# Optimization experiments

Measured on AMD Instinct MI355X. Metric: run time of the kernel, lower is better.

## Reference

```python
import jax, jax.numpy as jnp
import numpy as np

N_NODES = 50000
N_FEAT = 128
N_HIDDEN = 256
N_CLASSES = 1
N_EDGES = 800000


def gcn_layer(x, src, dst, W, b, n_nodes):
    """GCNConv: D^-1/2 (A + I) D^-1/2 X W + b, via gather-scatter over edges."""
    h = x @ W  # [N, out]
    # add self loops
    loop = jnp.arange(n_nodes, dtype=src.dtype)
    s = jnp.concatenate([src, loop])
    d = jnp.concatenate([dst, loop])
    deg = jax.ops.segment_sum(jnp.ones_like(d, dtype=h.dtype), d, num_segments=n_nodes)
    inv_sqrt = jax.lax.rsqrt(jnp.maximum(deg, 1.0))
    norm = inv_sqrt[s] * inv_sqrt[d]  # [E+N]
    msgs = h[s] * norm[:, None]       # gather: [E+N, out]
    out = jax.ops.segment_sum(msgs, d, num_segments=n_nodes)  # scatter-add
    return out + b


def setup_inputs() -> dict:
    key = jax.random.key(0)
    k1, k2, k3, k4 = jax.random.split(key, 4)
    x = jax.random.normal(k1, (N_NODES, N_FEAT), dtype=jnp.float32)
    edge_index = jax.random.randint(k2, (2, N_EDGES), 0, N_NODES, dtype=jnp.int32)
    s1 = 1.0 / np.sqrt(N_FEAT)
    s2 = 1.0 / np.sqrt(N_HIDDEN)
    W1 = jax.random.uniform(k3, (N_FEAT, N_HIDDEN), jnp.float32, -s1, s1)
    b1 = jnp.zeros((N_HIDDEN,), jnp.float32)
    W2 = jax.random.uniform(k4, (N_HIDDEN, N_CLASSES), jnp.float32, -s2, s2)
    b2 = jnp.zeros((N_CLASSES,), jnp.float32)
    return {"x": x, "edge_index": edge_index, "W1": W1, "b1": b1, "W2": W2, "b2": b2}


def reference(x, edge_index, W1, b1, W2, b2):
    src, dst = edge_index[0], edge_index[1]
    n = x.shape[0]
    h = gcn_layer(x, src, dst, W1, b1, n)
    h = jax.nn.relu(h)  # dropout=0.0 -> identity
    out = gcn_layer(h, src, dst, W2, b2, n)
    return out  # [N, n_classes]
```

## Files before the change

kernel.cpp:

```cpp
#include <hip/hip_runtime.h>

typedef unsigned int uint;
typedef unsigned short ushort;
typedef __attribute__((ext_vector_type(8))) short short8;
typedef __attribute__((ext_vector_type(4))) float f32x4;

#define CAP   64
#define BM16  16
#define STR   68
#define NPB   192
#define NBIN  261
#define CAPB  4096
#define EPB   4096

__device__ __forceinline__ float bf_lo(uint p) { return __uint_as_float(p << 16); }
__device__ __forceinline__ float bf_hi(uint p) { return __uint_as_float(p & 0xffff0000u); }
__device__ __forceinline__ uint rne_lo(uint u) { return (u + 0x7fffu + ((u >> 16) & 1u)) >> 16; }
__device__ __forceinline__ uint rne_hi(uint u) { return (u + 0x7fffu + ((u >> 16) & 1u)) & 0xffff0000u; }

__global__ __launch_bounds__(1024) void k_part(
    const int* __restrict__ src, const int* __restrict__ dst,
    int* __restrict__ binCnt, uint* __restrict__ binData, int E) {
  __shared__ int hist[NBIN];
  __shared__ int base[NBIN];
  int t = threadIdx.x;
  for (int i = t; i < NBIN; i += 1024) hist[i] = 0;
  __syncthreads();
  int s[4], d[4], b[4];
  bool v[4];
#pragma unroll
  for (int j = 0; j < 4; ++j) {
    int e = blockIdx.x * EPB + j * 1024 + t;
    v[j] = e < E;
    if (v[j]) {
      s[j] = src[e];
      d[j] = dst[e];
      b[j] = d[j] / NPB;
      atomicAdd(&hist[b[j]], 1);
    }
  }
  __syncthreads();
  for (int i = t; i < NBIN; i += 1024) {
    int h = hist[i];
    base[i] = h ? atomicAdd(&binCnt[i], h) : 0;
    hist[i] = 0;
  }
  __syncthreads();
#pragma unroll
  for (int j = 0; j < 4; ++j) {
    if (v[j]) {
      int r = atomicAdd(&hist[b[j]], 1);
      int idx = base[b[j]] + r;
      if (idx < CAPB)
        binData[b[j] * CAPB + idx] = (uint)s[j] | ((uint)d[j] << 16);
    }
  }
}

__global__ __launch_bounds__(1024) void k_bucketize(
    const uint* __restrict__ binData, const int* __restrict__ binCnt,
    ushort* __restrict__ col, int* __restrict__ cnt, int N) {
  __shared__ ushort col_l[NPB * CAP];
  __shared__ int cnt_l[NPB];
  int b = blockIdx.x, t = threadIdx.x;
  int lo = b * NPB;
  for (int i = t; i < NPB; i += 1024) cnt_l[i] = 0;
  __syncthreads();
  int m = min(binCnt[b], CAPB);
  const uint* bd = &binData[b * CAPB];
  for (int e = t; e < m; e += 1024) {
    uint pr = bd[e];
    int sv = pr & 0xffffu;
    int dl = (int)(pr >> 16) - lo;
    int p = atomicAdd(&cnt_l[dl], 1);
    if (p < CAP) col_l[dl * CAP + p] = (ushort)sv;
  }
  __syncthreads();
  int nh = min(NPB, N - lo);
  if (nh <= 0) return;
  for (int i = t; i < nh; i += 1024) cnt[lo + i] = cnt_l[i];
  uint* cg = (uint*)(col + (size_t)lo * CAP);
  const uint* cl = (const uint*)col_l;
  int nu = nh * (CAP / 2);
  for (int i = t; i < nu; i += 1024) cg[i] = cl[i];
}

__global__ void k_prep2(const float2* __restrict__ x2, const int* __restrict__ cnt,
                        uint* __restrict__ xs, float* __restrict__ inv,
                        const float* __restrict__ W1, uint* __restrict__ wpack,
                        int N, int nconv) {
  int gid = blockIdx.x * blockDim.x + threadIdx.x;
  if (gid < 4096) {
    int kk = gid >> 10, rem = gid & 1023, ntile = rem >> 6, ln = rem & 63;
    int quad = ln >> 4, nn = ntile * 16 + (ln & 15);
    uint d[4];
#pragma unroll
    for (int jp = 0; jp < 4; ++jp) {
      int k = kk * 32 + quad * 8 + 2 * jp;
      uint lov = rne_lo(__float_as_uint(W1[k * 256 + nn]));
      uint hiv = rne_hi(__float_as_uint(W1[(k + 1) * 256 + nn]));
      d[jp] = lov | hiv;
    }
    *(uint4*)&wpack[gid * 4] = make_uint4(d[0], d[1], d[2], d[3]);
  } else if (gid < 4096 + N) {
    int i = gid - 4096;
    inv[i] = rsqrtf((float)(cnt[i] + 1));
  } else if (gid < 4096 + N + nconv) {
    int cid = gid - 4096 - N;
    int node = cid >> 6;
    float invd = rsqrtf((float)(cnt[node] + 1));
    float2 f = x2[cid];
    xs[cid] = rne_lo(__float_as_uint(invd * f.x)) | rne_hi(__float_as_uint(invd * f.y));
  }
}

__global__ __launch_bounds__(256, 2) void k_agg_gemm(
    const uint* __restrict__ xs, const ushort* __restrict__ col,
    const int* __restrict__ cnt, const float* __restrict__ inv,
    const uint* __restrict__ wpack, const float* __restrict__ b1,
    const float* __restrict__ W2, float* __restrict__ cz, int N) {
  __shared__ uint As[BM16 * STR];
  __shared__ float red[64];
  int t = threadIdx.x, wave = t >> 6, lane = t & 63;
  int m0 = blockIdx.x * BM16;

  for (int rr = 0; rr < 4; ++rr) {
    int m = wave * 4 + rr;
    int node = m0 + m;
    float2 acc = make_float2(0.f, 0.f);
    if (node < N) {
      uint pd = xs[(size_t)node * 64 + lane];
      acc.x = bf_lo(pd);
      acc.y = bf_hi(pd);
      int e = min(cnt[node], CAP);
      int ce = (int)col[node * CAP + lane];
      int p = 0;
      for (; p + 15 < e; p += 16) {
        uint pv[16];
#pragma unroll
        for (int j = 0; j < 16; ++j) {
          int s = __shfl(ce, p + j);
          pv[j] = xs[(size_t)s * 64 + lane];
        }
#pragma unroll
        for (int j = 0; j < 16; ++j) { acc.x += bf_lo(pv[j]); acc.y += bf_hi(pv[j]); }
      }
      for (; p + 3 < e; p += 4) {
        uint pv[4];
#pragma unroll
        for (int j = 0; j < 4; ++j) {
          int s = __shfl(ce, p + j);
          pv[j] = xs[(size_t)s * 64 + lane];
        }
#pragma unroll
        for (int j = 0; j < 4; ++j) { acc.x += bf_lo(pv[j]); acc.y += bf_hi(pv[j]); }
      }
      for (; p < e; ++p) {
        int s = __shfl(ce, p);
        uint p0 = xs[(size_t)s * 64 + lane];
        acc.x += bf_lo(p0); acc.y += bf_hi(p0);
      }
      float invd = inv[node];
      acc.x *= invd;
      acc.y *= invd;
    }
    As[m * STR + lane] = rne_lo(__float_as_uint(acc.x)) | rne_hi(__float_as_uint(acc.y));
  }
  __syncthreads();

  int quad = lane >> 4, mrow = lane & 15;
  f32x4 acc[4];
#pragma unroll
  for (int nt = 0; nt < 4; ++nt) acc[nt] = (f32x4){0.f, 0.f, 0.f, 0.f};
#pragma unroll
  for (int kk = 0; kk < 4; ++kk) {
    short8 af = *(const short8*)&As[mrow * STR + kk * 16 + quad * 4];
#pragma unroll
    for (int nt = 0; nt < 4; ++nt) {
      int ntile = wave * 4 + nt;
      short8 bf = *(const short8*)&wpack[((kk * 16 + ntile) * 64 + lane) * 4];
      acc[nt] = __builtin_amdgcn_mfma_f32_16x16x32_bf16(af, bf, acc[nt], 0, 0, 0);
    }
  }

  float partial[4] = {0.f, 0.f, 0.f, 0.f};
#pragma unroll
  for (int nt = 0; nt < 4; ++nt) {
    int c = (wave * 4 + nt) * 16 + mrow;
    float b1c = b1[c], w2c = W2[c];
#pragma unroll
    for (int r = 0; r < 4; ++r) {
      float h = fmaxf(acc[nt][r] + b1c, 0.f);
      partial[r] = fmaf(h, w2c, partial[r]);
    }
  }
#pragma unroll
  for (int r = 0; r < 4; ++r) {
    float p = partial[r];
    p += __shfl_xor(p, 1); p += __shfl_xor(p, 2);
    p += __shfl_xor(p, 4); p += __shfl_xor(p, 8);
    if (mrow == 0) red[wave * 16 + quad * 4 + r] = p;
  }
  __syncthreads();
  if (t < 16) {
    int node = m0 + t;
    if (node < N) {
      float s = red[t] + red[16 + t] + red[32 + t] + red[48 + t];
      cz[node] = inv[node] * s;
    }
  }
}

__global__ void k_agg2(const ushort* __restrict__ col, const int* __restrict__ cnt,
                       const float* __restrict__ cz, const float* __restrict__ b2,
                       float* __restrict__ out, int N) {
  int g = blockIdx.x * blockDim.x + threadIdx.x;
  int node = g >> 2, q = g & 3;
  if (node >= N) return;
  int e = min(cnt[node], CAP);
  float acc = (q == 0) ? cz[node] : 0.f;
  const ushort* cp = &col[node * CAP];
  for (int p = q; p < e; p += 4) acc += cz[cp[p]];
  acc += __shfl_xor(acc, 1);
  acc += __shfl_xor(acc, 2);
  if (q == 0) out[node] = rsqrtf((float)(cnt[node] + 1)) * acc + b2[0];
}

extern "C" void kernel_launch(void* const* d_in, const int* in_sizes, int n_in,
                              void* d_out, int out_size, void* d_ws, size_t ws_size,
                              hipStream_t stream) {
  const float2* x2 = (const float2*)d_in[0];
  const int*    ei = (const int*)d_in[1];
  const float*  W1 = (const float*)d_in[2];
  const float*  b1 = (const float*)d_in[3];
  const float*  W2 = (const float*)d_in[4];
  const float*  b2 = (const float*)d_in[5];
  int N = in_sizes[0] / 128;
  int E = in_sizes[1] / 2;
  const int* src = ei;
  const int* dst = ei + E;
  float* out = (float*)d_out;

  char* w = (char*)d_ws;
  size_t o = 0;
  auto carve = [&](size_t bytes) { char* p = w + o; o += (bytes + 255) & ~(size_t)255; return p; };
  int*    binCnt  = (int*)   carve((size_t)NBIN * 4);
  int*    cnt     = (int*)   carve((size_t)N * 4);
  uint*   binData = (uint*)  carve((size_t)NBIN * CAPB * 4);
  ushort* col     = (ushort*)carve((size_t)N * CAP * 2);
  uint*   xs      = (uint*)  carve((size_t)N * 64 * 4);
  float*  inv     = (float*) carve((size_t)N * 4);
  uint*   wpack   = (uint*)  carve(16384 * 4);
  float*  cz      = (float*) carve((size_t)N * 4);

  hipMemsetAsync(binCnt, 0, (size_t)NBIN * sizeof(int), stream);

  int nblk_p = (E + EPB - 1) / EPB;
  k_part<<<nblk_p, 1024, 0, stream>>>(src, dst, binCnt, binData, E);

  k_bucketize<<<NBIN, 1024, 0, stream>>>(binData, binCnt, col, cnt, N);

  int nconv = N * 64;
  int tprep = 4096 + N + nconv;
  k_prep2<<<(tprep + 255) / 256, 256, 0, stream>>>(x2, cnt, xs, inv, W1, wpack, N, nconv);

  k_agg_gemm<<<(N + BM16 - 1) / BM16, 256, 0, stream>>>(
      xs, col, cnt, inv, wpack, b1, W2, cz, N);

  long long tot2 = (long long)N * 4;
  k_agg2<<<(int)((tot2 + 255) / 256), 256, 0, stream>>>(col, cnt, cz, b2, out, N);
}
```

Measured before the change: 144.3 us.

## Fold prep kernel into partition/bucketize and interleave gathers across four nodes

Removes the separate prep kernel. W1 packing moves into the edge-partition kernel, while the degree inverse and the scaled bf16 conversion of x move into the bucketize kernel, which already holds per-node counts in shared memory. The aggregation loop now gathers neighbours for all four of a wave's nodes together in chunks of eight, which keeps more loads in flight, and occupancy is raised to 3 blocks per CU. The cost is extra padded loads for nodes with uneven degree, more register pressure from the interleaving, and zeroing of the shared column buffer.

```diff
diff --git a/kernel.cpp b/kernel.cpp
--- a/kernel.cpp
+++ b/kernel.cpp
@@ -20,10 +20,27 @@
 
 __global__ __launch_bounds__(1024) void k_part(
     const int* __restrict__ src, const int* __restrict__ dst,
-    int* __restrict__ binCnt, uint* __restrict__ binData, int E) {
+    int* __restrict__ binCnt, uint* __restrict__ binData, int E,
+    const float* __restrict__ W1, uint* __restrict__ wpack) {
   __shared__ int hist[NBIN];
   __shared__ int base[NBIN];
   int t = threadIdx.x;
+
+  int gid = blockIdx.x * 1024 + t;
+  if (gid < 4096) {
+    int kk = gid >> 10, rem = gid & 1023, ntile = rem >> 6, ln = rem & 63;
+    int quad = ln >> 4, nn = ntile * 16 + (ln & 15);
+    uint d[4];
+#pragma unroll
+    for (int jp = 0; jp < 4; ++jp) {
+      int k = kk * 32 + quad * 8 + 2 * jp;
+      uint lov = rne_lo(__float_as_uint(W1[k * 256 + nn]));
+      uint hiv = rne_hi(__float_as_uint(W1[(k + 1) * 256 + nn]));
+      d[jp] = lov | hiv;
+    }
+    *(uint4*)&wpack[gid * 4] = make_uint4(d[0], d[1], d[2], d[3]);
+  }
+
   for (int i = t; i < NBIN; i += 1024) hist[i] = 0;
   __syncthreads();
   int s[4], d[4], b[4];
@@ -59,12 +76,15 @@
 
 __global__ __launch_bounds__(1024) void k_bucketize(
     const uint* __restrict__ binData, const int* __restrict__ binCnt,
-    ushort* __restrict__ col, int* __restrict__ cnt, int N) {
+    ushort* __restrict__ col, int* __restrict__ cnt, int N,
+    const float2* __restrict__ x2, uint* __restrict__ xs, float* __restrict__ inv) {
   __shared__ ushort col_l[NPB * CAP];
   __shared__ int cnt_l[NPB];
   int b = blockIdx.x, t = threadIdx.x;
   int lo = b * NPB;
   for (int i = t; i < NPB; i += 1024) cnt_l[i] = 0;
+  uint* clz = (uint*)col_l;
+  for (int i = t; i < NPB * (CAP / 2); i += 1024) clz[i] = 0;
   __syncthreads();
   int m = min(binCnt[b], CAPB);
   const uint* bd = &binData[b * CAPB];
@@ -78,43 +98,26 @@
   __syncthreads();
   int nh = min(NPB, N - lo);
   if (nh <= 0) return;
-  for (int i = t; i < nh; i += 1024) cnt[lo + i] = cnt_l[i];
+  for (int i = t; i < nh; i += 1024) {
+    int c = cnt_l[i];
+    cnt[lo + i] = c;
+    inv[lo + i] = rsqrtf((float)(c + 1));
+  }
   uint* cg = (uint*)(col + (size_t)lo * CAP);
   const uint* cl = (const uint*)col_l;
   int nu = nh * (CAP / 2);
   for (int i = t; i < nu; i += 1024) cg[i] = cl[i];
-}
-
-__global__ void k_prep2(const float2* __restrict__ x2, const int* __restrict__ cnt,
-                        uint* __restrict__ xs, float* __restrict__ inv,
-                        const float* __restrict__ W1, uint* __restrict__ wpack,
-                        int N, int nconv) {
-  int gid = blockIdx.x * blockDim.x + threadIdx.x;
-  if (gid < 4096) {
-    int kk = gid >> 10, rem = gid & 1023, ntile = rem >> 6, ln = rem & 63;
-    int quad = ln >> 4, nn = ntile * 16 + (ln & 15);
-    uint d[4];
-#pragma unroll
-    for (int jp = 0; jp < 4; ++jp) {
-      int k = kk * 32 + quad * 8 + 2 * jp;
-      uint lov = rne_lo(__float_as_uint(W1[k * 256 + nn]));
-      uint hiv = rne_hi(__float_as_uint(W1[(k + 1) * 256 + nn]));
-      d[jp] = lov | hiv;
-    }
-    *(uint4*)&wpack[gid * 4] = make_uint4(d[0], d[1], d[2], d[3]);
-  } else if (gid < 4096 + N) {
-    int i = gid - 4096;
-    inv[i] = rsqrtf((float)(cnt[i] + 1));
-  } else if (gid < 4096 + N + nconv) {
-    int cid = gid - 4096 - N;
-    int node = cid >> 6;
-    float invd = rsqrtf((float)(cnt[node] + 1));
-    float2 f = x2[cid];
-    xs[cid] = rne_lo(__float_as_uint(invd * f.x)) | rne_hi(__float_as_uint(invd * f.y));
-  }
-}
-
-__global__ __launch_bounds__(256, 2) void k_agg_gemm(
+  int nc = nh << 6;
+  const float2* xb = x2 + ((size_t)lo << 6);
+  uint* xo = xs + ((size_t)lo << 6);
+  for (int i = t; i < nc; i += 1024) {
+    float iv = rsqrtf((float)(cnt_l[i >> 6] + 1));
+    float2 f = xb[i];
+    xo[i] = rne_lo(__float_as_uint(iv * f.x)) | rne_hi(__float_as_uint(iv * f.y));
+  }
+}
+
+__global__ __launch_bounds__(256, 3) void k_agg_gemm(
     const uint* __restrict__ xs, const ushort* __restrict__ col,
     const int* __restrict__ cnt, const float* __restrict__ inv,
     const uint* __restrict__ wpack, const float* __restrict__ b1,
@@ -124,47 +127,56 @@
   int t = threadIdx.x, wave = t >> 6, lane = t & 63;
   int m0 = blockIdx.x * BM16;
 
-  for (int rr = 0; rr < 4; ++rr) {
-    int m = wave * 4 + rr;
-    int node = m0 + m;
-    float2 acc = make_float2(0.f, 0.f);
+  int e4[4], ce4[4];
+  float2 ac[4];
+  float invd[4];
+#pragma unroll
+  for (int r = 0; r < 4; ++r) {
+    int node = m0 + wave * 4 + r;
     if (node < N) {
       uint pd = xs[(size_t)node * 64 + lane];
-      acc.x = bf_lo(pd);
-      acc.y = bf_hi(pd);
-      int e = min(cnt[node], CAP);
-      int ce = (int)col[node * CAP + lane];
-      int p = 0;
-      for (; p + 15 < e; p += 16) {
-        uint pv[16];
-#pragma unroll
-        for (int j = 0; j < 16; ++j) {
-          int s = __shfl(ce, p + j);
-          pv[j] = xs[(size_t)s * 64 + lane];
+      ac[r].x = bf_lo(pd);
+      ac[r].y = bf_hi(pd);
+      e4[r] = min(cnt[node], CAP);
+      ce4[r] = (int)col[(size_t)node * CAP + lane];
+      invd[r] = inv[node];
+    } else {
+      e4[r] = 0; ce4[r] = 0; invd[r] = 0.f;
+      ac[r] = make_float2(0.f, 0.f);
+    }
+  }
+  int emax = max(max(e4[0], e4[1]), max(e4[2], e4[3]));
+  for (int p = 0; p < emax; p += 8) {
+    uint pv[4][8];
+#pragma unroll
+    for (int r = 0; r < 4; ++r) {
+      if (p < e4[r]) {
+#pragma unroll
+        for (int j = 0; j < 8; ++j) {
+          int s = __shfl(ce4[r], p + j);
+          pv[r][j] = xs[(size_t)s * 64 + lane];
         }
-#pragma unroll
-        for (int j = 0; j < 16; ++j) { acc.x += bf_lo(pv[j]); acc.y += bf_hi(pv[j]); }
       }
-      for (; p + 3 < e; p += 4) {
-        uint pv[4];
-#pragma unroll
-        for (int j = 0; j < 4; ++j) {
-          int s = __shfl(ce, p + j);
-          pv[j] = xs[(size_t)s * 64 + lane];
+    }
+#pragma unroll
+    for (int r = 0; r < 4; ++r) {
+      if (p < e4[r]) {
+        int lim = e4[r] - p;
+#pragma unroll
+        for (int j = 0; j < 8; ++j) {
+          uint v = (j < lim) ? pv[r][j] : 0u;
+          ac[r].x += bf_lo(v);
+          ac[r].y += bf_hi(v);
         }
-#pragma unroll
-        for (int j = 0; j < 4; ++j) { acc.x += bf_lo(pv[j]); acc.y += bf_hi(pv[j]); }
       }
-      for (; p < e; ++p) {
-        int s = __shfl(ce, p);
-        uint p0 = xs[(size_t)s * 64 + lane];
-        acc.x += bf_lo(p0); acc.y += bf_hi(p0);
-      }
-      float invd = inv[node];
-      acc.x *= invd;
-      acc.y *= invd;
-    }
-    As[m * STR + lane] = rne_lo(__float_as_uint(acc.x)) | rne_hi(__float_as_uint(acc.y));
+    }
+  }
+#pragma unroll
+  for (int r = 0; r < 4; ++r) {
+    float axx = ac[r].x * invd[r];
+    float ayy = ac[r].y * invd[r];
+    As[(wave * 4 + r) * STR + lane] =
+        rne_lo(__float_as_uint(axx)) | rne_hi(__float_as_uint(ayy));
   }
   __syncthreads();
 
@@ -256,13 +268,9 @@
   hipMemsetAsync(binCnt, 0, (size_t)NBIN * sizeof(int), stream);
 
   int nblk_p = (E + EPB - 1) / EPB;
-  k_part<<<nblk_p, 1024, 0, stream>>>(src, dst, binCnt, binData, E);
-
-  k_bucketize<<<NBIN, 1024, 0, stream>>>(binData, binCnt, col, cnt, N);
-
-  int nconv = N * 64;
-  int tprep = 4096 + N + nconv;
-  k_prep2<<<(tprep + 255) / 256, 256, 0, stream>>>(x2, cnt, xs, inv, W1, wpack, N, nconv);
+  k_part<<<nblk_p, 1024, 0, stream>>>(src, dst, binCnt, binData, E, W1, wpack);
+
+  k_bucketize<<<NBIN, 1024, 0, stream>>>(binData, binCnt, col, cnt, N, x2, xs, inv);
 
   k_agg_gemm<<<(N + BM16 - 1) / BM16, 256, 0, stream>>>(
       xs, col, cnt, inv, wpack, b1, W2, cz, N);
```

Result: no change. 147.2 us (+2.0%).
